# Performance work log

Hardware: AMD Instinct MI355X
Metric: run time of the kernel (lower is better)

The kernel has to match this reference:

```python
import jax, jax.numpy as jnp
import numpy as np
from jax import lax

DIM = 128      # per-head dim == channel dim of input
HEADS = 8
INNER = DIM * HEADS
KSZ = 3        # proj_kernel
PAD = KSZ // 2
B = 8
X = 4096       # sequence length
EPS = 1e-5     # BatchNorm eps
SCALE = DIM ** -0.5


def _dw_block(x, dw_w, bn_g, bn_b, bn_m, bn_v, pw_w, pad):
    """DepthWiseConv1d: depthwise conv -> eval-mode BN -> 1x1 conv (no bias).
    x: (n, dim, L); dw_w: (dim, 1, k); pw_w: (out, dim)."""
    dim = dw_w.shape[0]
    y = lax.conv_general_dilated(x, dw_w, (1,), [(pad, pad)],
                                 dimension_numbers=('NCH', 'OIH', 'NCH'),
                                 feature_group_count=dim)
    y = (y - bn_m[:, None]) * (bn_g[:, None] * lax.rsqrt(bn_v[:, None] + EPS)) + bn_b[:, None]
    return jnp.einsum('oi,nix->nox', pw_w, y)


def setup_inputs() -> dict:
    key = jax.random.key(0)
    ks = iter(jax.random.split(key, 40))
    d = {'x': jax.random.normal(next(ks), (B, DIM, X), dtype=jnp.float32)}
    for p in ('q', 'k', 'v'):
        d[p + '_dw'] = jax.random.normal(next(ks), (DIM, 1, KSZ), dtype=jnp.float32) * 0.3
        d[p + '_g'] = 1.0 + 0.1 * jax.random.normal(next(ks), (DIM,), dtype=jnp.float32)
        d[p + '_b'] = 0.1 * jax.random.normal(next(ks), (DIM,), dtype=jnp.float32)
        d[p + '_m'] = 0.1 * jax.random.normal(next(ks), (DIM,), dtype=jnp.float32)
        d[p + '_v'] = jax.random.uniform(next(ks), (DIM,), dtype=jnp.float32, minval=0.5, maxval=1.5)
        d[p + '_pw'] = jax.random.normal(next(ks), (INNER, DIM), dtype=jnp.float32) * (DIM ** -0.5)
    # gating DWConv (dim -> dim, kernel 1, no bias)
    d['gt_dw'] = jax.random.normal(next(ks), (DIM, 1, 1), dtype=jnp.float32) * 0.3
    d['gt_g'] = 1.0 + 0.1 * jax.random.normal(next(ks), (DIM,), dtype=jnp.float32)
    d['gt_b'] = 0.1 * jax.random.normal(next(ks), (DIM,), dtype=jnp.float32)
    d['gt_m'] = 0.1 * jax.random.normal(next(ks), (DIM,), dtype=jnp.float32)
    d['gt_v'] = jax.random.uniform(next(ks), (DIM,), dtype=jnp.float32, minval=0.5, maxval=1.5)
    d['gt_pw'] = jax.random.normal(next(ks), (DIM, DIM), dtype=jnp.float32) * (DIM ** -0.5)
    # to_out 1x1 conv (inner -> dim) with bias
    d['out_w'] = jax.random.normal(next(ks), (DIM, INNER), dtype=jnp.float32) * (INNER ** -0.5)
    d['out_b'] = 0.1 * jax.random.normal(next(ks), (DIM,), dtype=jnp.float32)
    return d


def _split_heads(t):
    # (b, h*d, x) -> (b*h, x, d)
    return t.reshape(B, HEADS, DIM, X).transpose(0, 1, 3, 2).reshape(B * HEADS, X, DIM)


def reference(x, q_dw, q_g, q_b, q_m, q_v, q_pw,
              k_dw, k_g, k_b, k_m, k_v, k_pw,
              v_dw, v_g, v_b, v_m, v_v, v_pw,
              gt_dw, gt_g, gt_b, gt_m, gt_v, gt_pw,
              out_w, out_b):
    q = _split_heads(_dw_block(x, q_dw, q_g, q_b, q_m, q_v, q_pw, PAD))  # (n, x, d)
    k = _split_heads(_dw_block(x, k_dw, k_g, k_b, k_m, k_v, k_pw, PAD))
    v = _split_heads(_dw_block(x, v_dw, v_g, v_b, v_m, v_v, v_pw, PAD))
    # k <- q^T @ softmax(k, axis=-1) * scale : (n, d, d)
    kat = jnp.einsum('nxd,nxe->nde', q, jax.nn.softmax(k, axis=-1)) * SCALE
    # gate: sigmoid(DWConv(q^T)^T) * v
    g_out = _dw_block(q.transpose(0, 2, 1), gt_dw, gt_g, gt_b, gt_m, gt_v, gt_pw, 0)  # (n, d, x)
    gate = jax.nn.sigmoid(g_out.transpose(0, 2, 1)) * v                  # (n, x, d)
    out = jnp.einsum('nxd,nde->nxe', v, kat) + gate                      # (n, x, d)
    out = out.reshape(B, HEADS, X, DIM).transpose(0, 1, 3, 2).reshape(B, INNER, X)
    return jnp.einsum('oi,nix->nox', out_w, out) + out_b[:, None]        # (b, dim, x)
```

## Files before the change

kernel.cpp:

```cpp
#include <hip/hip_runtime.h>
#include <hip/hip_bf16.h>

#define DIMC   128
#define HEADS  8
#define BATCH  8
#define XLEN   4096
#define NHEAD  64
#define EPSV   1e-5f
#define SCALEF 0.08838834764831845f
#define TX     64

typedef __attribute__((ext_vector_type(8))) short bf16x8;
typedef __attribute__((ext_vector_type(4))) float f32x4;
#define MFMA(a,b,c) __builtin_amdgcn_mfma_f32_16x16x32_bf16((a),(b),(c),0,0,0)
#define LDW(tbl, kt, nt) (*(const bf16x8*)&(tbl)[(((kt) * 8 + (nt)) * 64 + l) * 8])

__device__ __forceinline__ short f2bf(float f) {
  union { float f; unsigned u; } v; v.f = f;
  return (short)((v.u + 0x7fffu + ((v.u >> 16) & 1u)) >> 16);
}
__device__ __forceinline__ float bf2f(short h) {
  union { unsigned u; float f; } v; v.u = ((unsigned)(unsigned short)h) << 16;
  return v.f;
}
__device__ __forceinline__ unsigned pk2(float a, float b) {
  return (unsigned)(unsigned short)f2bf(a) | ((unsigned)(unsigned short)f2bf(b) << 16);
}

__device__ __forceinline__ bf16x8 ldY(const short* Y, int row, int kcb) {
  return *(const bf16x8*)((const char*)Y + row*256 + (kcb ^ ((row&7)<<4)));
}

__global__ void k_prep1(const float* dw0, const float* g0, const float* b0, const float* m0, const float* v0,
                        const float* dw1, const float* g1, const float* b1, const float* m1, const float* v1,
                        const float* dw2, const float* g2, const float* b2, const float* m2, const float* v2,
                        const float* gt_pw, const float* gt_dw, const float* gt_g,
                        const float* gt_b, const float* gt_m, const float* gt_v,
                        float* __restrict__ dwf, float* __restrict__ bfl,
                        float* __restrict__ Gt, float* __restrict__ c0) {
  int p = blockIdx.x, c = threadIdx.x;
  if (p < 3) {
    const float* dw = p == 0 ? dw0 : p == 1 ? dw1 : dw2;
    const float* g  = p == 0 ? g0  : p == 1 ? g1  : g2;
    const float* bb = p == 0 ? b0  : p == 1 ? b1  : b2;
    const float* m  = p == 0 ? m0  : p == 1 ? m1  : m2;
    const float* vv = p == 0 ? v0  : p == 1 ? v1  : v2;
    float a = g[c] * rsqrtf(vv[c] + EPSV);
    dwf[(p * DIMC + c) * 3 + 0] = dw[c * 3 + 0] * a;
    dwf[(p * DIMC + c) * 3 + 1] = dw[c * 3 + 1] * a;
    dwf[(p * DIMC + c) * 3 + 2] = dw[c * 3 + 2] * a;
    bfl[p * DIMC + c] = bb[c] - m[c] * a;
  } else {
    int d = c;
    float s = 0.f;
    for (int i = 0; i < DIMC; ++i) {
      float a  = gt_g[i] * rsqrtf(gt_v[i] + EPSV);
      float w1 = gt_dw[i] * a;
      float w0 = gt_b[i] - gt_m[i] * a;
      float pw = gt_pw[d * DIMC + i];
      Gt[i * DIMC + d] = pw * w1;
      s += pw * w0;
    }
    c0[d] = s;
  }
}

__global__ void k_wg(const float* __restrict__ q_pw, const float* __restrict__ Gt,
                     float* __restrict__ WgF) {
  const int h = blockIdx.x, cb = blockIdx.y, t = threadIdx.x;
  const int c = cb * 16 + (t >> 4);
  const int e0 = (t & 15) * 8;
  float acc[8] = {0.f,0.f,0.f,0.f,0.f,0.f,0.f,0.f};
  for (int d = 0; d < DIMC; ++d) {
    float wq = q_pw[((size_t)(h * DIMC + d)) * DIMC + c];
    const float* gr = Gt + d * DIMC + e0;
    #pragma unroll
    for (int j = 0; j < 8; ++j) acc[j] += wq * gr[j];
  }
  float* out = WgF + ((size_t)h * DIMC + c) * DIMC + e0;
  #pragma unroll
  for (int j = 0; j < 8; ++j) out[j] = acc[j];
}

__global__ void k_pack(const float* __restrict__ q_pw, const float* __restrict__ k_pw,
                       const float* __restrict__ v_pw, const float* __restrict__ out_w,
                       const float* __restrict__ WgF,
                       short* __restrict__ Wpk, short* __restrict__ Opk,
                       short* __restrict__ Gpk) {
  const int blk = blockIdx.x, t = threadIdx.x;
  if (blk < 24) {
    const int p = blk / 8, h = blk & 7;
    const float* pw = p == 0 ? q_pw : p == 1 ? k_pw : v_pw;
    short* dst = Wpk + (size_t)((p * 8 + h) * 2 + 0) * 16384;
    for (int s = t; s < 2048; s += 256) {
      const int l = s & 63, kt = (s >> 6) >> 3, nt = (s >> 6) & 7;
      const int o = h * DIMC + nt * 16 + (l & 15);
      const int cb = kt * 32 + (l >> 4) * 8;
      #pragma unroll
      for (int j = 0; j < 8; ++j)
        dst[s * 8 + j] = f2bf(pw[(size_t)o * DIMC + cb + j]);
    }
  } else if (blk < 32) {
    const int h = blk - 24;
    short* dst = Opk + (size_t)(h * 2 + 0) * 16384;
    for (int s = t; s < 2048; s += 256) {
      const int l = s & 63, mt = (s >> 6) >> 2, kt = (s >> 6) & 3;
      const int o = mt * 16 + (l & 15);
      const int ib = h * DIMC + kt * 32 + (l >> 4) * 8;
      #pragma unroll
      for (int j = 0; j < 8; ++j)
        dst[s * 8 + j] = f2bf(out_w[(size_t)o * (DIMC * HEADS) + ib + j]);
    }
  } else {
    const int h = blk - 32;
    const float* src = WgF + (size_t)h * 16384;
    short* dst = Gpk + (size_t)h * 16384;
    for (int s = t; s < 2048; s += 256) {
      const int l = s & 63, kt = (s >> 6) >> 3, nt = (s >> 6) & 7;
      const int cb = kt * 32 + (l >> 4) * 8, e = nt * 16 + (l & 15);
      #pragma unroll
      for (int j = 0; j < 8; ++j) dst[s * 8 + j] = f2bf(src[(size_t)(cb + j) * DIMC + e]);
    }
  }
}

__global__ __launch_bounds__(256) void k_red(const short* __restrict__ part16,
                                             short* __restrict__ katpk, int splits) {
  __shared__ float sm[DIMC * DIMC];
  const int n = blockIdx.x, t = threadIdx.x;
  for (int i0 = t * 8; i0 < DIMC * DIMC; i0 += 256 * 8) {
    float a[8] = {0.f,0.f,0.f,0.f,0.f,0.f,0.f,0.f};
    for (int s8 = 0; s8 < splits; ++s8) {
      bf16x8 pv = *(const bf16x8*)&part16[((size_t)(s8 * NHEAD + n)) * 16384 + i0];
      #pragma unroll
      for (int j = 0; j < 8; ++j) a[j] += bf2f(pv[j]);
    }
    #pragma unroll
    for (int j = 0; j < 8; ++j) sm[i0 + j] = a[j] * SCALEF;
  }
  __syncthreads();
  short* dst = katpk + (size_t)n * 16384;
  for (int s = t; s < 2048; s += 256) {
    const int l = s & 63, kt = (s >> 6) >> 3, nt = (s >> 6) & 7;
    const int db = kt * 32 + (l >> 4) * 8, e = nt * 16 + (l & 15);
    #pragma unroll
    for (int j = 0; j < 8; ++j) dst[s * 8 + j] = f2bf(sm[(db + j) * DIMC + e]);
  }
}

__device__ __forceinline__ void stage2(const float* __restrict__ x,
    const float* __restrict__ dwf, const float* __restrict__ bfl,
    int b, int xg0, int t, short* Y0, short* Y1, int p0, int p1)
{
  const int xl = t & 63, cg = t >> 6;
  const int xg = xg0 + xl;
  #pragma unroll
  for (int i = 0; i < 16; ++i) {
    const int c = 2 * (cg + 4 * i);
    float v0[2], v1[2];
    #pragma unroll
    for (int u = 0; u < 2; ++u) {
      const int cc = c + u;
      const float* xr = x + ((size_t)b * DIMC + cc) * XLEN + xg;
      float xm = (xg > 0) ? xr[-1] : 0.f;
      float xc = xr[0];
      float xp = (xg < XLEN - 1) ? xr[1] : 0.f;
      const float* d0 = dwf + (p0 * DIMC + cc) * 3;
      const float* d1 = dwf + (p1 * DIMC + cc) * 3;
      v0[u] = xm * d0[0] + xc * d0[1] + xp * d0[2] + bfl[p0 * DIMC + cc];
      v1[u] = xm * d1[0] + xc * d1[1] + xp * d1[2] + bfl[p1 * DIMC + cc];
    }
    const unsigned off = xl * 256 + ((c * 2) ^ ((xl & 7) << 4));
    *(unsigned*)((char*)Y0 + off) = pk2(v0[0], v0[1]);
    *(unsigned*)((char*)Y1 + off) = pk2(v1[0], v1[1]);
  }
}

__global__ __launch_bounds__(256) void k_proj(
    const float* __restrict__ x, const float* __restrict__ dwf,
    const float* __restrict__ bfl, const short* __restrict__ Wpk,
    short* __restrict__ qT, short* __restrict__ sT, int b)
{
  __shared__ __align__(16) short Yq[TX * 128], Yk[TX * 128];
  __shared__ __align__(16) short QT[128 * TX], ST[128 * TX];
  const int t = threadIdx.x, w = t >> 6, l = t & 63;
  const int l15 = l & 15, lq = l >> 4;
  const int h = blockIdx.y;
  const int x0 = blockIdx.x * TX;

  stage2(x, dwf, bfl, b, x0, t, Yq, Yk, 0, 1);
  __syncthreads();

  const short* WqHi = Wpk + (size_t)((0 * 8 + h) * 2 + 0) * 16384;
  const short* WkHi = Wpk + (size_t)((1 * 8 + h) * 2 + 0) * 16384;

  f32x4 qa[8];

  #pragma unroll
  for (int j = 0; j < 8; ++j) qa[j] = {0.f, 0.f, 0.f, 0.f};
  {
    bf16x8 a0 = ldY(Yq, w * 16 + l15, 0 * 64 + lq * 16);
    bf16x8 a1 = ldY(Yq, w * 16 + l15, 1 * 64 + lq * 16);
    bf16x8 a2 = ldY(Yq, w * 16 + l15, 2 * 64 + lq * 16);
    bf16x8 a3 = ldY(Yq, w * 16 + l15, 3 * 64 + lq * 16);
    bf16x8 h0[8], h1[8];
    #pragma unroll
    for (int nt = 0; nt < 8; ++nt) h0[nt] = LDW(WqHi, 0, nt);
    #pragma unroll
    for (int nt = 0; nt < 8; ++nt) h1[nt] = LDW(WqHi, 1, nt);
    #pragma unroll
    for (int nt = 0; nt < 8; ++nt) qa[nt] = MFMA(a0, h0[nt], qa[nt]);
    #pragma unroll
    for (int nt = 0; nt < 8; ++nt) h0[nt] = LDW(WqHi, 2, nt);
    #pragma unroll
    for (int nt = 0; nt < 8; ++nt) qa[nt] = MFMA(a1, h1[nt], qa[nt]);
    #pragma unroll
    for (int nt = 0; nt < 8; ++nt) h1[nt] = LDW(WqHi, 3, nt);
    #pragma unroll
    for (int nt = 0; nt < 8; ++nt) qa[nt] = MFMA(a2, h0[nt], qa[nt]);
    #pragma unroll
    for (int nt = 0; nt < 8; ++nt) qa[nt] = MFMA(a3, h1[nt], qa[nt]);
  }
  #pragma unroll
  for (int nt = 0; nt < 8; ++nt) {
    const int d = nt * 16 + l15;
    #pragma unroll
    for (int rp = 0; rp < 2; ++rp) {
      const int x2 = w * 16 + lq * 4 + rp * 2;
      *(unsigned*)((char*)QT + d * 128 + ((x2 * 2) ^ ((d & 7) << 4))) =
          pk2(qa[nt][rp * 2], qa[nt][rp * 2 + 1]);
    }
  }

  #pragma unroll
  for (int j = 0; j < 8; ++j) qa[j] = {0.f, 0.f, 0.f, 0.f};
  {
    bf16x8 a0 = ldY(Yk, w * 16 + l15, 0 * 64 + lq * 16);
    bf16x8 a1 = ldY(Yk, w * 16 + l15, 1 * 64 + lq * 16);
    bf16x8 a2 = ldY(Yk, w * 16 + l15, 2 * 64 + lq * 16);
    bf16x8 a3 = ldY(Yk, w * 16 + l15, 3 * 64 + lq * 16);
    bf16x8 h0[8], h1[8];
    #pragma unroll
    for (int nt = 0; nt < 8; ++nt) h0[nt] = LDW(WkHi, 0, nt);
    #pragma unroll
    for (int nt = 0; nt < 8; ++nt) h1[nt] = LDW(WkHi, 1, nt);
    #pragma unroll
    for (int nt = 0; nt < 8; ++nt) qa[nt] = MFMA(a0, h0[nt], qa[nt]);
    #pragma unroll
    for (int nt = 0; nt < 8; ++nt) h0[nt] = LDW(WkHi, 2, nt);
    #pragma unroll
    for (int nt = 0; nt < 8; ++nt) qa[nt] = MFMA(a1, h1[nt], qa[nt]);
    #pragma unroll
    for (int nt = 0; nt < 8; ++nt) h1[nt] = LDW(WkHi, 3, nt);
    #pragma unroll
    for (int nt = 0; nt < 8; ++nt) qa[nt] = MFMA(a2, h0[nt], qa[nt]);
    #pragma unroll
    for (int nt = 0; nt < 8; ++nt) qa[nt] = MFMA(a3, h1[nt], qa[nt]);
  }
  float inv[4];
  #pragma unroll
  for (int r = 0; r < 4; ++r) {
    float m = qa[0][r];
    #pragma unroll
    for (int nt = 1; nt < 8; ++nt) m = fmaxf(m, qa[nt][r]);
    m = fmaxf(m, __shfl_xor(m, 1)); m = fmaxf(m, __shfl_xor(m, 2));
    m = fmaxf(m, __shfl_xor(m, 4)); m = fmaxf(m, __shfl_xor(m, 8));
    float s = 0.f;
    #pragma unroll
    for (int nt = 0; nt < 8; ++nt) { float e = __expf(qa[nt][r] - m); qa[nt][r] = e; s += e; }
    s += __shfl_xor(s, 1); s += __shfl_xor(s, 2); s += __shfl_xor(s, 4); s += __shfl_xor(s, 8);
    inv[r] = 1.f / s;
  }
  #pragma unroll
  for (int nt = 0; nt < 8; ++nt) {
    const int e = nt * 16 + l15;
    #pragma unroll
    for (int rp = 0; rp < 2; ++rp) {
      const int x2 = w * 16 + lq * 4 + rp * 2;
      *(unsigned*)((char*)ST + e * 128 + ((x2 * 2) ^ ((e & 7) << 4))) =
          pk2(qa[nt][rp * 2] * inv[rp * 2], qa[nt][rp * 2 + 1] * inv[rp * 2 + 1]);
    }
  }
  __syncthreads();

  {
    const int r = t >> 1, half = t & 1;
    const size_t row = ((size_t)h * DIMC + r) * XLEN + x0 + half * 32;
    #pragma unroll
    for (int i = 0; i < 4; ++i) {
      const int off = r * 128 + (((half * 64) + i * 16) ^ ((r & 7) << 4));
      *(int4*)(qT + row + i * 8) = *(const int4*)((const char*)QT + off);
      *(int4*)(sT + row + i * 8) = *(const int4*)((const char*)ST + off);
    }
  }
}

__global__ __launch_bounds__(256) void k_katg(
    const short* __restrict__ qT, const short* __restrict__ sT,
    short* __restrict__ part16, int b)
{
  __shared__ __align__(16) short QL[128 * 128];
  __shared__ __align__(16) short SL[16 * 128];
  const int t = threadIdx.x, w = t >> 6, l = t & 63;
  const int l15 = l & 15, lq = l >> 4;
  const int h = blockIdx.y, eq = blockIdx.z;
  const int n = b * HEADS + h;
  const int xspan = XLEN / gridDim.x;

  f32x4 ka[2];
  ka[0] = {0.f, 0.f, 0.f, 0.f};
  ka[1] = {0.f, 0.f, 0.f, 0.f};

  for (int ch = 0; ch < xspan / 128; ++ch) {
    const int xl0 = blockIdx.x * xspan + ch * 128;
    __syncthreads();
    #pragma unroll
    for (int R = 0; R < 8; ++R) {
      const int idx = R * 256 + t;
      const int d = idx >> 4, c = idx & 15;
      const size_t rb = (((size_t)h * DIMC + d) * XLEN + xl0) * 2;
      *(int4*)((char*)QL + idx * 16) =
          *(const int4*)((const char*)qT + rb + ((c * 16) ^ ((d & 7) << 4)));
    }
    {
      const int idx = t;
      const int er = idx >> 4, c = idx & 15;
      const size_t rb = (((size_t)h * DIMC + eq * 16 + er) * XLEN + xl0) * 2;
      *(int4*)((char*)SL + idx * 16) =
          *(const int4*)((const char*)sT + rb + ((c * 16) ^ ((er & 7) << 4)));
    }
    __syncthreads();
    #pragma unroll
    for (int kt2 = 0; kt2 < 4; ++kt2) {
      bf16x8 a0 = ldY(QL, w * 32 + l15,      kt2 * 64 + lq * 16);
      bf16x8 a1 = ldY(QL, w * 32 + 16 + l15, kt2 * 64 + lq * 16);
      bf16x8 bs = ldY(SL, l15, kt2 * 64 + lq * 16);
      ka[0] = MFMA(a0, bs, ka[0]);
      ka[1] = MFMA(a1, bs, ka[1]);
    }
  }
  short* dst = part16 + ((size_t)(blockIdx.x * NHEAD + n)) * 16384;
  #pragma unroll
  for (int mt = 0; mt < 2; ++mt)
    #pragma unroll
    for (int r = 0; r < 4; ++r) {
      const int d = w * 32 + mt * 16 + lq * 4 + r;
      const int e = eq * 16 + l15;
      dst[d * DIMC + e] = f2bf(ka[mt][r]);
    }
}

__global__ __launch_bounds__(256) void k_out11(
    const float* __restrict__ x, const float* __restrict__ dwf,
    const float* __restrict__ bfl, const short* __restrict__ Wpk,
    const short* __restrict__ Gpk, const short* __restrict__ katpk,
    const short* __restrict__ Opk, const float* __restrict__ c0,
    const float* __restrict__ outb, float* __restrict__ outp)
{
  __shared__ __align__(16) short Yq[TX * 128], Yv[TX * 128];
  __shared__ __align__(16) short Vx[TX * 128], Tn[TX * 128];
  const int t = threadIdx.x, w = t >> 6, l = t & 63;
  const int l15 = l & 15, lq = l >> 4;
  const int b = blockIdx.y;
  const int x0 = blockIdx.x * TX;

  f32x4 oacc[2][4];
  #pragma unroll
  for (int i = 0; i < 2; ++i)
    #pragma unroll
    for (int j = 0; j < 4; ++j) oacc[i][j] = {0.f, 0.f, 0.f, 0.f};
  float c0v[8];
  #pragma unroll
  for (int nt = 0; nt < 8; ++nt) c0v[nt] = c0[nt * 16 + l15];

  stage2(x, dwf, bfl, b, x0, t, Yq, Yv, 0, 2);
  __syncthreads();

  for (int h = 0; h < HEADS; ++h) {
    const int n = b * HEADS + h;
    const short* WvHi = Wpk + (size_t)((2 * 8 + h) * 2 + 0) * 16384;
    const short* Wg   = Gpk + (size_t)h * 16384;
    const short* Kp   = katpk + (size_t)n * 16384;
    const short* OHi  = Opk + (size_t)(h * 2 + 0) * 16384;

    bf16x8 P0[8], P1[8], Q0[8], Q1[8];
    #pragma unroll
    for (int i = 0; i < 8; ++i) P0[i] = LDW(WvHi, 0, i);
    #pragma unroll
    for (int i = 0; i < 8; ++i) P1[i] = LDW(WvHi, 1, i);
    #pragma unroll
    for (int i = 0; i < 8; ++i) Q0[i] = LDW(WvHi, 2, i);
    #pragma unroll
    for (int i = 0; i < 8; ++i) Q1[i] = LDW(WvHi, 3, i);

    f32x4 va[8];
    #pragma unroll
    for (int j = 0; j < 8; ++j) va[j] = {0.f, 0.f, 0.f, 0.f};
    {
      bf16x8 a = ldY(Yv, w * 16 + l15, 0 * 64 + lq * 16);
      #pragma unroll
      for (int nt = 0; nt < 8; ++nt) va[nt] = MFMA(a, P0[nt], va[nt]);
    }
    #pragma unroll
    for (int i = 0; i < 8; ++i) P0[i] = LDW(Wg, 0, i);
    {
      bf16x8 a = ldY(Yv, w * 16 + l15, 1 * 64 + lq * 16);
      #pragma unroll
      for (int nt = 0; nt < 8; ++nt) va[nt] = MFMA(a, P1[nt], va[nt]);
    }
    #pragma unroll
    for (int i = 0; i < 8; ++i) P1[i] = LDW(Wg, 1, i);
    {
      bf16x8 a = ldY(Yv, w * 16 + l15, 2 * 64 + lq * 16);
      #pragma unroll
      for (int nt = 0; nt < 8; ++nt) va[nt] = MFMA(a, Q0[nt], va[nt]);
    }
    #pragma unroll
    for (int i = 0; i < 8; ++i) Q0[i] = LDW(Wg, 2, i);
    {
      bf16x8 a = ldY(Yv, w * 16 + l15, 3 * 64 + lq * 16);
      #pragma unroll
      for (int nt = 0; nt < 8; ++nt) va[nt] = MFMA(a, Q1[nt], va[nt]);
    }
    #pragma unroll
    for (int i = 0; i < 8; ++i) Q1[i] = LDW(Wg, 3, i);

    #pragma unroll
    for (int nt = 0; nt < 8; ++nt) {
      const int dd = nt * 16 + l15;
      #pragma unroll
      for (int r = 0; r < 4; ++r) {
        const int xr = w * 16 + lq * 4 + r;
        *(short*)((char*)Vx + xr * 256 + ((dd * 2) ^ ((xr & 7) << 4))) = f2bf(va[nt][r]);
      }
    }

    f32x4 ga[8];
    #pragma unroll
    for (int j = 0; j < 8; ++j) ga[j] = {0.f, 0.f, 0.f, 0.f};
    {
      bf16x8 a = ldY(Yq, w * 16 + l15, 0 * 64 + lq * 16);
      #pragma unroll
      for (int nt = 0; nt < 8; ++nt) ga[nt] = MFMA(a, P0[nt], ga[nt]);
    }
    #pragma unroll
    for (int i = 0; i < 8; ++i) P0[i] = LDW(Kp, 0, i);
    {
      bf16x8 a = ldY(Yq, w * 16 + l15, 1 * 64 + lq * 16);
      #pragma unroll
      for (int nt = 0; nt < 8; ++nt) ga[nt] = MFMA(a, P1[nt], ga[nt]);
    }
    #pragma unroll
    for (int i = 0; i < 8; ++i) P1[i] = LDW(Kp, 1, i);
    {
      bf16x8 a = ldY(Yq, w * 16 + l15, 2 * 64 + lq * 16);
      #pragma unroll
      for (int nt = 0; nt < 8; ++nt) ga[nt] = MFMA(a, Q0[nt], ga[nt]);
    }
    #pragma unroll
    for (int i = 0; i < 8; ++i) Q0[i] = LDW(Kp, 2, i);
    {
      bf16x8 a = ldY(Yq, w * 16 + l15, 3 * 64 + lq * 16);
      #pragma unroll
      for (int nt = 0; nt < 8; ++nt) ga[nt] = MFMA(a, Q1[nt], ga[nt]);
    }
    #pragma unroll
    for (int i = 0; i < 8; ++i) Q1[i] = LDW(Kp, 3, i);

    #pragma unroll
    for (int nt = 0; nt < 8; ++nt)
      #pragma unroll
      for (int r = 0; r < 4; ++r)
        ga[nt][r] = 1.f / (1.f + __expf(-(ga[nt][r] + c0v[nt])));

    f32x4 kv[8];
    #pragma unroll
    for (int j = 0; j < 8; ++j) kv[j] = {0.f, 0.f, 0.f, 0.f};
    {
      bf16x8 a = ldY(Vx, w * 16 + l15, 0 * 64 + lq * 16);
      #pragma unroll
      for (int nt = 0; nt < 8; ++nt) kv[nt] = MFMA(a, P0[nt], kv[nt]);
    }
    #pragma unroll
    for (int i = 0; i < 8; ++i)
      P0[i] = (*(const bf16x8*)&OHi[((((w * 2 + (i >> 2)) * 4 + (i & 3))) * 64 + l) * 8]);
    {
      bf16x8 a = ldY(Vx, w * 16 + l15, 1 * 64 + lq * 16);
      #pragma unroll
      for (int nt = 0; nt < 8; ++nt) kv[nt] = MFMA(a, P1[nt], kv[nt]);
    }
    {
      bf16x8 a = ldY(Vx, w * 16 + l15, 2 * 64 + lq * 16);
      #pragma unroll
      for (int nt = 0; nt < 8; ++nt) kv[nt] = MFMA(a, Q0[nt], kv[nt]);
    }
    {
      bf16x8 a = ldY(Vx, w * 16 + l15, 3 * 64 + lq * 16);
      #pragma unroll
      for (int nt = 0; nt < 8; ++nt) kv[nt] = MFMA(a, Q1[nt], kv[nt]);
    }

    #pragma unroll
    for (int nt = 0; nt < 8; ++nt) {
      const int e = nt * 16 + l15;
      #pragma unroll
      for (int r = 0; r < 4; ++r) {
        const int xr = w * 16 + lq * 4 + r;
        float vv = bf2f(*(const short*)((const char*)Vx + xr * 256 + ((e * 2) ^ ((xr & 7) << 4))));
        *(short*)((char*)Tn + xr * 256 + ((e * 2) ^ ((xr & 7) << 4))) =
            f2bf(kv[nt][r] + ga[nt][r] * vv);
      }
    }
    __syncthreads();

    #pragma unroll
    for (int kt = 0; kt < 4; ++kt) {
      #pragma unroll
      for (int nt4 = 0; nt4 < 4; ++nt4) {
        bf16x8 bt = ldY(Tn, nt4 * 16 + l15, kt * 64 + lq * 16);
        oacc[0][nt4] = MFMA(P0[0 * 4 + kt], bt, oacc[0][nt4]);
        oacc[1][nt4] = MFMA(P0[1 * 4 + kt], bt, oacc[1][nt4]);
      }
    }
    __syncthreads();
  }
  #pragma unroll
  for (int mt = 0; mt < 2; ++mt) {
    #pragma unroll
    for (int nt4 = 0; nt4 < 4; ++nt4) {
      #pragma unroll
      for (int r = 0; r < 4; ++r) {
        const int o = w * 32 + mt * 16 + lq * 4 + r;
        const int xx = x0 + nt4 * 16 + l15;
        outp[((size_t)b * DIMC + o) * XLEN + xx] = oacc[mt][nt4][r] + outb[o];
      }
    }
  }
}

extern "C" void kernel_launch(void* const* d_in, const int* in_sizes, int n_in,
                              void* d_out, int out_size, void* d_ws, size_t ws_size,
                              hipStream_t stream) {
  (void)in_sizes; (void)n_in; (void)out_size;
  const float* x = (const float*)d_in[0];

  char* ws = (char*)d_ws;
  short* katpk = (short*)(ws);
  short* Wpk   = (short*)(ws + 2097152);
  short* Opk   = (short*)(ws + 3670016);
  short* Gpk   = (short*)(ws + 4194304);
  float* WgF   = (float*)(ws + 4456448);
  float* Gt    = (float*)(ws + 4980736);
  float* c0    = (float*)(ws + 5046272);
  float* dwf   = (float*)(ws + 5046784);
  float* bfl   = (float*)(ws + 5051392);
  constexpr size_t BASE = 5052928;
  const int splits = (ws_size >= (size_t)38607360) ? 8 : 4;
  short* part16 = (short*)(ws + BASE);
  short* qT = (short*)(ws + BASE + (size_t)splits * 2097152);
  short* sT = (short*)((char*)qT + 8388608);
  if (ws_size < (size_t)30218752) return;

  k_prep1<<<4, 128, 0, stream>>>(
      (const float*)d_in[1],  (const float*)d_in[2],  (const float*)d_in[3],
      (const float*)d_in[4],  (const float*)d_in[5],
      (const float*)d_in[7],  (const float*)d_in[8],  (const float*)d_in[9],
      (const float*)d_in[10], (const float*)d_in[11],
      (const float*)d_in[13], (const float*)d_in[14], (const float*)d_in[15],
      (const float*)d_in[16], (const float*)d_in[17],
      (const float*)d_in[24], (const float*)d_in[19], (const float*)d_in[20],
      (const float*)d_in[21], (const float*)d_in[22], (const float*)d_in[23],
      dwf, bfl, Gt, c0);

  k_wg<<<dim3(8, 8), 256, 0, stream>>>((const float*)d_in[6], Gt, WgF);

  k_pack<<<40, 256, 0, stream>>>((const float*)d_in[6], (const float*)d_in[12],
                                 (const float*)d_in[18], (const float*)d_in[25],
                                 WgF, Wpk, Opk, Gpk);

  for (int b = 0; b < BATCH; ++b) {
    k_proj<<<dim3(XLEN / TX, HEADS), 256, 0, stream>>>(x, dwf, bfl, Wpk, qT, sT, b);
    k_katg<<<dim3(splits, HEADS, 8), 256, 0, stream>>>(qT, sT, part16, b);
  }
  k_red<<<NHEAD, 256, 0, stream>>>(part16, katpk, splits);
  k_out11<<<dim3(XLEN / TX, BATCH), 256, 0, stream>>>(x, dwf, bfl, Wpk, Gpk, katpk,
                                                      Opk, c0, (const float*)d_in[26],
                                                      (float*)d_out);
}
```

Baseline: 399.5 us.

## Process two batches per proj/katg launch and compact workspace layout

Removes the unused hi-half slots in the packed weight buffers and compacts the workspace, placing WgF in the area later reused by part16. When the workspace is large enough, k_proj and k_katg now cover two batches per launch (16 head slots), halving the launch count and doubling grid size, while katg splits drop from 8 to 2. Fewer splits mean longer serial loops per katg block, but each launch has more blocks. The smaller-workspace paths keep the old one-batch behaviour.

```diff
diff --git a/kernel.cpp b/kernel.cpp
--- a/kernel.cpp
+++ b/kernel.cpp
@@ -91,7 +91,7 @@
   if (blk < 24) {
     const int p = blk / 8, h = blk & 7;
     const float* pw = p == 0 ? q_pw : p == 1 ? k_pw : v_pw;
-    short* dst = Wpk + (size_t)((p * 8 + h) * 2 + 0) * 16384;
+    short* dst = Wpk + (size_t)(p * 8 + h) * 16384;
     for (int s = t; s < 2048; s += 256) {
       const int l = s & 63, kt = (s >> 6) >> 3, nt = (s >> 6) & 7;
       const int o = h * DIMC + nt * 16 + (l & 15);
@@ -102,7 +102,7 @@
     }
   } else if (blk < 32) {
     const int h = blk - 24;
-    short* dst = Opk + (size_t)(h * 2 + 0) * 16384;
+    short* dst = Opk + (size_t)h * 16384;
     for (int s = t; s < 2048; s += 256) {
       const int l = s & 63, mt = (s >> 6) >> 2, kt = (s >> 6) & 3;
       const int o = mt * 16 + (l & 15);
@@ -179,20 +179,21 @@
 __global__ __launch_bounds__(256) void k_proj(
     const float* __restrict__ x, const float* __restrict__ dwf,
     const float* __restrict__ bfl, const short* __restrict__ Wpk,
-    short* __restrict__ qT, short* __restrict__ sT, int b)
+    short* __restrict__ qT, short* __restrict__ sT, int b0)
 {
   __shared__ __align__(16) short Yq[TX * 128], Yk[TX * 128];
   __shared__ __align__(16) short QT[128 * TX], ST[128 * TX];
   const int t = threadIdx.x, w = t >> 6, l = t & 63;
   const int l15 = l & 15, lq = l >> 4;
-  const int h = blockIdx.y;
+  const int slot = blockIdx.y;
+  const int b = b0 + (slot >> 3), h = slot & 7;
   const int x0 = blockIdx.x * TX;
 
   stage2(x, dwf, bfl, b, x0, t, Yq, Yk, 0, 1);
   __syncthreads();
 
-  const short* WqHi = Wpk + (size_t)((0 * 8 + h) * 2 + 0) * 16384;
-  const short* WkHi = Wpk + (size_t)((1 * 8 + h) * 2 + 0) * 16384;
+  const short* WqHi = Wpk + (size_t)(0 * 8 + h) * 16384;
+  const short* WkHi = Wpk + (size_t)(1 * 8 + h) * 16384;
 
   f32x4 qa[8];
 
@@ -285,7 +286,7 @@
 
   {
     const int r = t >> 1, half = t & 1;
-    const size_t row = ((size_t)h * DIMC + r) * XLEN + x0 + half * 32;
+    const size_t row = ((size_t)slot * DIMC + r) * XLEN + x0 + half * 32;
     #pragma unroll
     for (int i = 0; i < 4; ++i) {
       const int off = r * 128 + (((half * 64) + i * 16) ^ ((r & 7) << 4));
@@ -297,14 +298,13 @@
 
 __global__ __launch_bounds__(256) void k_katg(
     const short* __restrict__ qT, const short* __restrict__ sT,
-    short* __restrict__ part16, int b)
+    short* __restrict__ part16, int n0)
 {
   __shared__ __align__(16) short QL[128 * 128];
   __shared__ __align__(16) short SL[16 * 128];
   const int t = threadIdx.x, w = t >> 6, l = t & 63;
   const int l15 = l & 15, lq = l >> 4;
-  const int h = blockIdx.y, eq = blockIdx.z;
-  const int n = b * HEADS + h;
+  const int slot = blockIdx.y, eq = blockIdx.z;
   const int xspan = XLEN / gridDim.x;
 
   f32x4 ka[2];
@@ -318,14 +318,14 @@
     for (int R = 0; R < 8; ++R) {
       const int idx = R * 256 + t;
       const int d = idx >> 4, c = idx & 15;
-      const size_t rb = (((size_t)h * DIMC + d) * XLEN + xl0) * 2;
+      const size_t rb = (((size_t)slot * DIMC + d) * XLEN + xl0) * 2;
       *(int4*)((char*)QL + idx * 16) =
           *(const int4*)((const char*)qT + rb + ((c * 16) ^ ((d & 7) << 4)));
     }
     {
       const int idx = t;
       const int er = idx >> 4, c = idx & 15;
-      const size_t rb = (((size_t)h * DIMC + eq * 16 + er) * XLEN + xl0) * 2;
+      const size_t rb = (((size_t)slot * DIMC + eq * 16 + er) * XLEN + xl0) * 2;
       *(int4*)((char*)SL + idx * 16) =
           *(const int4*)((const char*)sT + rb + ((c * 16) ^ ((er & 7) << 4)));
     }
@@ -339,7 +339,7 @@
       ka[1] = MFMA(a1, bs, ka[1]);
     }
   }
-  short* dst = part16 + ((size_t)(blockIdx.x * NHEAD + n)) * 16384;
+  short* dst = part16 + ((size_t)(blockIdx.x * NHEAD + n0 + slot)) * 16384;
   #pragma unroll
   for (int mt = 0; mt < 2; ++mt)
     #pragma unroll
@@ -378,10 +378,10 @@
 
   for (int h = 0; h < HEADS; ++h) {
     const int n = b * HEADS + h;
-    const short* WvHi = Wpk + (size_t)((2 * 8 + h) * 2 + 0) * 16384;
+    const short* WvHi = Wpk + (size_t)(2 * 8 + h) * 16384;
     const short* Wg   = Gpk + (size_t)h * 16384;
     const short* Kp   = katpk + (size_t)n * 16384;
-    const short* OHi  = Opk + (size_t)(h * 2 + 0) * 16384;
+    const short* OHi  = Opk + (size_t)h * 16384;
 
     bf16x8 P0[8], P1[8], Q0[8], Q1[8];
     #pragma unroll
@@ -547,19 +547,27 @@
   char* ws = (char*)d_ws;
   short* katpk = (short*)(ws);
   short* Wpk   = (short*)(ws + 2097152);
-  short* Opk   = (short*)(ws + 3670016);
-  short* Gpk   = (short*)(ws + 4194304);
-  float* WgF   = (float*)(ws + 4456448);
-  float* Gt    = (float*)(ws + 4980736);
-  float* c0    = (float*)(ws + 5046272);
-  float* dwf   = (float*)(ws + 5046784);
-  float* bfl   = (float*)(ws + 5051392);
-  constexpr size_t BASE = 5052928;
-  const int splits = (ws_size >= (size_t)38607360) ? 8 : 4;
+  short* Opk   = (short*)(ws + 2883584);
+  short* Gpk   = (short*)(ws + 3145728);
+  float* Gt    = (float*)(ws + 3407872);
+  float* c0    = (float*)(ws + 3473408);
+  float* dwf   = (float*)(ws + 3473920);
+  float* bfl   = (float*)(ws + 3478528);
+  constexpr size_t BASE = 3480064;
+  float* WgF   = (float*)(ws + BASE);
+
+  int BPL, splits;
+  if (ws_size >= (size_t)(BASE + 2u*2097152 + 2u*8388608 + 2u*8388608 + 16777216)) {
+    BPL = 2; splits = 2;
+  } else if (ws_size >= (size_t)(BASE + 8u*2097152 + 8388608 + 8388608)) {
+    BPL = 1; splits = 8;
+  } else {
+    BPL = 1; splits = 4;
+  }
   short* part16 = (short*)(ws + BASE);
   short* qT = (short*)(ws + BASE + (size_t)splits * 2097152);
-  short* sT = (short*)((char*)qT + 8388608);
-  if (ws_size < (size_t)30218752) return;
+  short* sT = (short*)((char*)qT + (size_t)BPL * 8388608);
+  if (ws_size < (size_t)28645888) return;
 
   k_prep1<<<4, 128, 0, stream>>>(
       (const float*)d_in[1],  (const float*)d_in[2],  (const float*)d_in[3],
@@ -578,9 +586,11 @@
                                  (const float*)d_in[18], (const float*)d_in[25],
                                  WgF, Wpk, Opk, Gpk);
 
-  for (int b = 0; b < BATCH; ++b) {
-    k_proj<<<dim3(XLEN / TX, HEADS), 256, 0, stream>>>(x, dwf, bfl, Wpk, qT, sT, b);
-    k_katg<<<dim3(splits, HEADS, 8), 256, 0, stream>>>(qT, sT, part16, b);
+  for (int b0 = 0; b0 < BATCH; b0 += BPL) {
+    k_proj<<<dim3(XLEN / TX, HEADS * BPL), 256, 0, stream>>>(x, dwf, bfl, Wpk,
+                                                             qT, sT, b0);
+    k_katg<<<dim3(splits, HEADS * BPL, 8), 256, 0, stream>>>(qT, sT, part16,
+                                                             b0 * HEADS);
   }
   k_red<<<NHEAD, 256, 0, stream>>>(part16, katpk, splits);
   k_out11<<<dim3(XLEN / TX, BATCH), 256, 0, stream>>>(x, dwf, bfl, Wpk, Gpk, katpk,
```

After: 361.6 us. -9.5%, faster.
